# Performance work log

Measured on AMD Instinct MI355X. Metric: run time of the kernel, lower is better.

## Reference

```python
import jax, jax.numpy as jnp
import numpy as np

D_MODEL = 2048
N_HEAD = 16
HEAD_DIM = D_MODEL // N_HEAD
SCALE = 1.0 / (HEAD_DIM ** 0.5)


def setup_inputs() -> dict:
    key = jax.random.key(0)
    kx, kq, kk, kv, ko = jax.random.split(key, 5)
    std = 1.0 / np.sqrt(D_MODEL)
    return {
        "x": jax.random.normal(kx, (2, 2048, D_MODEL), dtype=jnp.float32),
        "w_q": jax.random.normal(kq, (D_MODEL, D_MODEL), dtype=jnp.float32) * std,
        "w_k": jax.random.normal(kk, (D_MODEL, D_MODEL), dtype=jnp.float32) * std,
        "w_v": jax.random.normal(kv, (D_MODEL, D_MODEL), dtype=jnp.float32) * std,
        "w_o": jax.random.normal(ko, (D_MODEL, D_MODEL), dtype=jnp.float32) * std,
    }


def reference(x, w_q, w_k, w_v, w_o):
    b, s, d = x.shape
    # nn.Linear(d,d,bias=False): y = x @ W^T, weights stored [out, in]
    def proj(w):
        y = jnp.einsum("bsd,ed->bse", x, w)
        return y.reshape(b, s, N_HEAD, HEAD_DIM).transpose(0, 2, 1, 3)  # [b,h,s,hd]
    q, k, v = proj(w_q), proj(w_k), proj(w_v)
    scores = jnp.einsum("bhqd,bhkd->bhqk", q, k) * SCALE  # [b,h,s,s]
    probs = jax.nn.softmax(scores, axis=-1)
    attn = jnp.einsum("bhqk,bhkd->bhqd", probs, v)
    attn = attn.transpose(0, 2, 1, 3).reshape(b, s, d)
    return jnp.einsum("bsd,ed->bse", attn, w_o)
```

## Files before the change

### kernel.cpp

```cpp
#include <hip/hip_runtime.h>

#define D_MODEL 2048
#define SEQ 2048
#define BATCH 2
#define NH 16
#define HD 128
#define MTOT 4096
#define NQKV 6144
#define QSTRIDE 4096

static constexpr float SCALE_LOG2E = 0.08838834764831845f * 1.4426950408889634f;

typedef __bf16 bf16x8 __attribute__((ext_vector_type(8)));
typedef _Float16 f16x4 __attribute__((ext_vector_type(4)));
typedef float f32x4 __attribute__((ext_vector_type(4)));

__device__ inline unsigned short f2bf(float f) {
  unsigned int u = __builtin_bit_cast(unsigned int, f);
  u += 0x7fffu + ((u >> 16) & 1u);
  return (unsigned short)(u >> 16);
}

__device__ inline float fast_exp2(float x) {
#if __has_builtin(__builtin_amdgcn_exp2f)
  return __builtin_amdgcn_exp2f(x);
#else
  return exp2f(x);
#endif
}

__device__ inline void gload_lds16(const void* g, void* s) {
  __builtin_amdgcn_global_load_lds(
      (__attribute__((address_space(1))) void*)g,
      (__attribute__((address_space(3))) void*)s, 16, 0, 0);
}

__global__ __launch_bounds__(256) void cvt_all(
    const float* __restrict__ x, const float* __restrict__ wq,
    const float* __restrict__ wk, const float* __restrict__ wv,
    const float* __restrict__ wo, unsigned short* __restrict__ xb,
    unsigned short* __restrict__ wqkv, unsigned short* __restrict__ wob) {
  const int y = blockIdx.y;
  const float* src;
  unsigned short* dst;
  int n4;
  if (y == 0) { src = x; dst = xb; n4 = MTOT * D_MODEL / 4; }
  else if (y == 4) { src = wo; dst = wob; n4 = D_MODEL * D_MODEL / 4; }
  else {
    src = (y == 1) ? wq : (y == 2) ? wk : wv;
    dst = wqkv + (size_t)(y - 1) * D_MODEL * D_MODEL;
    n4 = D_MODEL * D_MODEL / 4;
  }
  int i = blockIdx.x * 256 + threadIdx.x;
  if (i < n4) {
    float4 v = ((const float4*)src)[i];
    ushort4 o;
    o.x = f2bf(v.x); o.y = f2bf(v.y); o.z = f2bf(v.z); o.w = f2bf(v.w);
    ((ushort4*)dst)[i] = o;
  }
}

#define GEMM_SETUP(Aptr, Bptr)                                                 \
  const int tid = threadIdx.x;                                                 \
  const int lane = tid & 63;                                                   \
  const int wave = tid >> 6;                                                   \
  const int quad = lane >> 4;                                                  \
  const int l15 = lane & 15;                                                   \
  const int wm = wave >> 1;                                                    \
  const int wn = wave & 1;                                                     \
  const unsigned short* Ag =                                                   \
      (Aptr) + (size_t)(m0 + wave * 8 + (lane >> 3)) * 2048 +                  \
      (size_t)(((lane & 7) ^ (lane >> 3)) * 8);                                \
  const unsigned short* Bg =                                                   \
      (Bptr) + (size_t)(n0 + wave * 8 + (lane >> 3)) * 2048 +                  \
      (size_t)(((lane & 7) ^ (lane >> 3)) * 8);                                \
  char* sd = smem + wave * 1024;                                               \
  const int arow0 = (wm * 64 + l15) * 128;                                     \
  const int brow0 = (wn * 64 + l15) * 128;                                     \
  const int sk0 = ((quad) ^ (l15 & 7)) * 16;                                   \
  const int sk1 = ((4 + quad) ^ (l15 & 7)) * 16;                               \
  f32x4 acc[4][4] = {};

#define SA(tt, u, NB)                                                          \
  gload_lds16(Ag + (size_t)(u) * 64 * 2048 + (tt) * 64,                        \
              sd + (NB) * 49152 + (u) * 8192)
#define SB(tt, u, NB)                                                          \
  gload_lds16(Bg + (size_t)(u) * 64 * 2048 + (tt) * 64,                        \
              sd + (NB) * 49152 + 32768 + (u) * 8192)

#define RDA(dst, mi, CB)                                                       \
  dst[0] = *(const bf16x8*)(smem + (CB) * 49152 + arow0 + (mi) * 2048 + sk0);  \
  dst[1] = *(const bf16x8*)(smem + (CB) * 49152 + arow0 + (mi) * 2048 + sk1);
#define RDB(ni, CB)                                                            \
  bfr[ni][0] =                                                                 \
      *(const bf16x8*)(smem + (CB) * 49152 + 32768 + brow0 + (ni) * 2048 + sk0); \
  bfr[ni][1] =                                                                 \
      *(const bf16x8*)(smem + (CB) * 49152 + 32768 + brow0 + (ni) * 2048 + sk1);

#define MM2(mi, areg)                                                          \
  _Pragma("unroll") for (int ni_ = 0; ni_ < 4; ni_++) {                        \
    acc[mi][ni_] = __builtin_amdgcn_mfma_f32_16x16x32_bf16(                    \
        areg[0], bfr[ni_][0], acc[mi][ni_], 0, 0, 0);                          \
    acc[mi][ni_] = __builtin_amdgcn_mfma_f32_16x16x32_bf16(                    \
        areg[1], bfr[ni_][1], acc[mi][ni_], 0, 0, 0);                          \
  }

#define TILE(t, CB, NB, DOSTAGE, VMN)                                          \
  {                                                                            \
    bf16x8 af0[2], af1[2], af2[2], af3[2], bfr[4][2];                          \
    RDA(af0, 0, CB); RDA(af1, 1, CB);                                          \
    RDB(0, CB); RDB(1, CB); RDB(2, CB); RDB(3, CB);                            \
    if (DOSTAGE) { SA((t) + 2, 0, NB); SA((t) + 2, 1, NB); SB((t) + 2, 0, NB); } \
    __builtin_amdgcn_s_barrier();                                              \
    asm volatile("s_waitcnt lgkmcnt(0)" ::: "memory");                         \
    __builtin_amdgcn_sched_barrier(0);                                         \
    __builtin_amdgcn_s_setprio(1);                                             \
    MM2(0, af0); MM2(1, af1);                                                  \
    __builtin_amdgcn_s_setprio(0);                                             \
    __builtin_amdgcn_s_barrier();                                              \
    RDA(af2, 2, CB); RDA(af3, 3, CB);                                          \
    if (DOSTAGE) { SA((t) + 2, 2, NB); SA((t) + 2, 3, NB); SB((t) + 2, 1, NB); } \
    __builtin_amdgcn_s_barrier();                                              \
    asm volatile("s_waitcnt lgkmcnt(0)" ::: "memory");                         \
    __builtin_amdgcn_sched_barrier(0);                                         \
    __builtin_amdgcn_s_setprio(1);                                             \
    MM2(2, af2); MM2(3, af3);                                                  \
    __builtin_amdgcn_s_setprio(0);                                             \
    asm volatile("s_waitcnt vmcnt(" #VMN ")" ::: "memory");                    \
    __builtin_amdgcn_s_barrier();                                              \
  }

#define GEMM_KLOOP()                                                           \
  SA(0, 0, 0); SA(0, 1, 0); SA(0, 2, 0); SA(0, 3, 0); SB(0, 0, 0); SB(0, 1, 0);\
  SA(1, 0, 1); SA(1, 1, 1); SA(1, 2, 1); SA(1, 3, 1); SB(1, 0, 1); SB(1, 1, 1);\
  asm volatile("s_waitcnt vmcnt(6)" ::: "memory");                             \
  __builtin_amdgcn_s_barrier();                                                \
  for (int t = 0; t < 30; t += 3) {                                            \
    TILE(t + 0, 0, 2, 1, 6);                                                   \
    TILE(t + 1, 1, 0, 1, 6);                                                   \
    TILE(t + 2, 2, 1, 1, 6);                                                   \
  }                                                                            \
  TILE(30, 0, 2, 0, 0);                                                        \
  TILE(31, 1, 0, 0, 0);

__global__ __launch_bounds__(512, 2) void gemm_qkv(
    const unsigned short* __restrict__ A, const unsigned short* __restrict__ B,
    unsigned short* __restrict__ QK, unsigned short* __restrict__ Vt) {
  extern __shared__ __align__(16) char smem[];
  const int bid = blockIdx.x;
  const int wgid = (bid & 7) * 96 + (bid >> 3);
  const int tm = wgid / 48;
  const int tn = wgid - tm * 48;
  const int m0 = tm * 256;
  const int n0 = tn * 128;
  GEMM_SETUP(A, B);
  GEMM_KLOOP();

  if (n0 < 4096) {
#pragma unroll
    for (int mi = 0; mi < 4; mi++)
#pragma unroll
      for (int ni = 0; ni < 4; ni++) {
        const int mm = m0 + wm * 64 + mi * 16 + quad * 4;
        const int nn = n0 + wn * 64 + ni * 16 + l15;
#pragma unroll
        for (int r = 0; r < 4; r++)
          QK[(size_t)(mm + r) * QSTRIDE + nn] = f2bf(acc[mi][ni][r]);
      }
  } else {
    asm volatile("s_waitcnt vmcnt(0)" ::: "memory");
    __builtin_amdgcn_s_barrier();
    unsigned short* T = (unsigned short*)smem;
    const int h = (n0 - 4096) >> 7;
    const int bb = m0 >> 11;
    const int sbase = m0 & (SEQ - 1);
#pragma unroll
    for (int mi = 0; mi < 4; mi++)
#pragma unroll
      for (int ni = 0; ni < 4; ni++) {
        const int d = wn * 64 + ni * 16 + l15;
        const int s = wm * 64 + mi * 16 + quad * 4;
        f16x4 hv;
#pragma unroll
        for (int r = 0; r < 4; r++) hv[r] = (_Float16)acc[mi][ni][r];
        *(f16x4*)(T + d * 264 + s) = hv;
      }
    __builtin_amdgcn_s_barrier();
    const int d = tid >> 2;
    const int sc = (tid & 3) * 64;
    const size_t vrow = ((size_t)(bb * NH + h) * HD + d) * SEQ + sbase + sc;
#pragma unroll
    for (int j = 0; j < 8; j++) {
      float4 c4 = *(const float4*)(T + d * 264 + sc + j * 8);
      *(float4*)(Vt + vrow + j * 8) = c4;
    }
  }
}

__global__ __launch_bounds__(512, 2) void gemm_out(
    const unsigned short* __restrict__ A, const unsigned short* __restrict__ B,
    float* __restrict__ C) {
  extern __shared__ __align__(16) char smem[];
  const int bid = blockIdx.x;
  const int wgid = (bid & 7) * 32 + (bid >> 3);
  const int tm = wgid >> 4;
  const int tn = wgid & 15;
  const int m0 = tm * 256;
  const int n0 = tn * 128;
  GEMM_SETUP(A, B);
  GEMM_KLOOP();

#pragma unroll
  for (int mi = 0; mi < 4; mi++)
#pragma unroll
    for (int ni = 0; ni < 4; ni++) {
      const int mm = m0 + wm * 64 + mi * 16 + quad * 4;
      const int nn = n0 + wn * 64 + ni * 16 + l15;
#pragma unroll
      for (int r = 0; r < 4; r++)
        C[(size_t)(mm + r) * D_MODEL + nn] = acc[mi][ni][r];
    }
}

__global__ __launch_bounds__(256, 2) void flash_attn(
    const unsigned short* __restrict__ QK, const unsigned short* __restrict__ Vt,
    unsigned short* __restrict__ Og) {
  __shared__ __align__(16) unsigned short Ks[2][64 * 128];
  __shared__ __align__(16) unsigned short Vs[2][128 * 64];
  const int tid = threadIdx.x;
  const int lane = tid & 63;
  const int wave = tid >> 6;
  const int quad = lane >> 4;
  const int l15 = lane & 15;
  const int id = blockIdx.x;
  const int xr = id & 7;
  const int kk = id >> 3;
  const int bh = xr * 4 + (kk >> 4);
  const int b = bh >> 4, h = bh & 15;
  const int q0 = (kk & 15) * 128;

  const size_t kbase = (size_t)(b * SEQ) * QSTRIDE + D_MODEL + h * HD;
  const size_t vbase = (size_t)bh * HD * SEQ;

  bf16x8 qf[2][4];
#pragma unroll
  for (int t = 0; t < 2; t++)
#pragma unroll
    for (int kc = 0; kc < 4; kc++)
      qf[t][kc] = *(const bf16x8*)(QK + (size_t)(b * SEQ + q0 + wave * 32 + t * 16 + l15) * QSTRIDE +
                                   h * HD + kc * 32 + quad * 8);

  const unsigned short* kg[4];
  const unsigned short* vg[4];
  int klofs[4], vlofs[4];
#pragma unroll
  for (int i = 0; i < 4; i++) {
    int krow = wave * 16 + i * 4 + quad;
    int kc_ = l15 ^ (i * 4 + quad);
    kg[i] = QK + kbase + (size_t)krow * QSTRIDE + kc_ * 8;
    klofs[i] = (wave * 16 + i * 4) * 128;
    int vrow = wave * 32 + i * 8 + (lane >> 3);
    int vc_ = (lane & 7) ^ (lane >> 3);
    vg[i] = Vt + vbase + (size_t)vrow * SEQ + vc_ * 8;
    vlofs[i] = (wave * 32 + i * 8) * 64;
  }

#pragma unroll
  for (int i = 0; i < 4; i++) gload_lds16(kg[i], &Ks[0][klofs[i]]);
#pragma unroll
  for (int i = 0; i < 4; i++) gload_lds16(vg[i], &Vs[0][vlofs[i]]);
#pragma unroll
  for (int i = 0; i < 4; i++) { kg[i] += 64 * QSTRIDE; vg[i] += 64; }
  __builtin_amdgcn_s_waitcnt(0);
  __syncthreads();

  float lsum[2] = {0.f, 0.f};
  f32x4 Oa[2][8] = {};

  for (int it = 0; it < SEQ / 64; ++it) {
    const int cur = it & 1;
    if (it < SEQ / 64 - 1) {
#pragma unroll
      for (int i = 0; i < 4; i++) gload_lds16(kg[i], &Ks[cur ^ 1][klofs[i]]);
#pragma unroll
      for (int i = 0; i < 4; i++) gload_lds16(vg[i], &Vs[cur ^ 1][vlofs[i]]);
#pragma unroll
      for (int i = 0; i < 4; i++) { kg[i] += 64 * QSTRIDE; vg[i] += 64; }
    }

    const unsigned short* kb = &Ks[cur][0];
    f32x4 sacc[2][4] = {};
#pragma unroll
    for (int js = 0; js < 4; js++)
#pragma unroll
      for (int kc = 0; kc < 4; kc++) {
        bf16x8 kf = *(const bf16x8*)(kb + (js * 16 + l15) * 128 + (((kc * 4 + quad) ^ l15) * 8));
        sacc[0][js] = __builtin_amdgcn_mfma_f32_16x16x32_bf16(kf, qf[0][kc], sacc[0][js], 0, 0, 0);
        sacc[1][js] = __builtin_amdgcn_mfma_f32_16x16x32_bf16(kf, qf[1][kc], sacc[1][js], 0, 0, 0);
      }

    f16x4 pb[2][4];
#pragma unroll
    for (int t = 0; t < 2; t++)
#pragma unroll
      for (int js = 0; js < 4; js++)
#pragma unroll
        for (int r = 0; r < 4; r++) {
          float p = fast_exp2(sacc[t][js][r] * SCALE_LOG2E);
          lsum[t] += p;
          pb[t][js][r] = (_Float16)p;
        }

    const unsigned short* vb_ = &Vs[cur][0];
#pragma unroll
    for (int jt = 0; jt < 8; jt++)
#pragma unroll
      for (int js = 0; js < 4; js++) {
        f16x4 vf = *(const f16x4*)(vb_ + (jt * 16 + l15) * 64 +
                                   (((js * 2 + (quad >> 1)) ^ (lane & 7)) * 8) + (quad & 1) * 4);
        Oa[0][jt] = __builtin_amdgcn_mfma_f32_16x16x16f16(vf, pb[0][js], Oa[0][jt], 0, 0, 0);
        Oa[1][jt] = __builtin_amdgcn_mfma_f32_16x16x16f16(vf, pb[1][js], Oa[1][jt], 0, 0, 0);
      }

    __builtin_amdgcn_s_waitcnt(0);
    __syncthreads();
  }

  float inv[2];
#pragma unroll
  for (int t = 0; t < 2; t++) {
    float s = lsum[t];
    s += __shfl_xor(s, 16);
    s += __shfl_xor(s, 32);
    inv[t] = 1.0f / s;
  }

#pragma unroll
  for (int t = 0; t < 2; t++) {
    const size_t rowbase = (size_t)(b * SEQ + q0 + wave * 32 + t * 16 + l15) * D_MODEL + h * HD;
#pragma unroll
    for (int jt = 0; jt < 8; jt++) {
      ushort4 o;
      o.x = f2bf(Oa[t][jt][0] * inv[t]);
      o.y = f2bf(Oa[t][jt][1] * inv[t]);
      o.z = f2bf(Oa[t][jt][2] * inv[t]);
      o.w = f2bf(Oa[t][jt][3] * inv[t]);
      *(ushort4*)(Og + rowbase + jt * 16 + quad * 4) = o;
    }
  }
}

extern "C" void kernel_launch(void* const* d_in, const int* in_sizes, int n_in,
                              void* d_out, int out_size, void* d_ws, size_t ws_size,
                              hipStream_t stream) {
  const float* x = (const float*)d_in[0];
  const float* wq = (const float*)d_in[1];
  const float* wk = (const float*)d_in[2];
  const float* wv = (const float*)d_in[3];
  const float* wo = (const float*)d_in[4];
  float* out = (float*)d_out;
  char* ws = (char*)d_ws;
  const size_t MB = 1u << 20;
  if (ws_size < 96 * MB) return;

  unsigned short* xb = (unsigned short*)(ws);
  unsigned short* wqkv = (unsigned short*)(ws + 16 * MB);
  unsigned short* wob = (unsigned short*)(ws + 40 * MB);
  unsigned short* QKb = (unsigned short*)(ws + 48 * MB);
  unsigned short* Vtb = (unsigned short*)(ws + 80 * MB);
  unsigned short* Ab = xb;

  static int lds_set = 0;
  if (!lds_set) {
    hipFuncSetAttribute((const void*)gemm_qkv,
                        hipFuncAttributeMaxDynamicSharedMemorySize, 147456);
    hipFuncSetAttribute((const void*)gemm_out,
                        hipFuncAttributeMaxDynamicSharedMemorySize, 147456);
    lds_set = 1;
  }

  cvt_all<<<dim3(8192, 5), 256, 0, stream>>>(x, wq, wk, wv, wo, xb, wqkv, wob);

  gemm_qkv<<<768, 512, 147456, stream>>>(xb, wqkv, QKb, Vtb);

  flash_attn<<<512, 256, 0, stream>>>(QKb, Vtb, Ab);

  gemm_out<<<256, 512, 147456, stream>>>(Ab, wob, out);
}
```

Baseline: 359.9 us.

## Split QKV GEMM into QK and V kernels with new tile shapes

Replaces the single fused QKV GEMM (256x128 tiles, 768 blocks) with two kernels. gemm_qk uses 256x256 tiles and a double-buffered schedule with 8x4 accumulators per wave. gemm_v and gemm_out use 128x256 tiles with a triple-buffered schedule. Larger tiles raise operand reuse per LDS load and improve arithmetic intensity. In exchange there is higher register pressure, an extra kernel launch, and grids of 256 blocks that may leave some compute units less well balanced.

```diff
diff --git a/kernel.cpp b/kernel.cpp
--- a/kernel.cpp
+++ b/kernel.cpp
@@ -34,6 +34,15 @@
       (__attribute__((address_space(1))) void*)g,
       (__attribute__((address_space(3))) void*)s, 16, 0, 0);
 }
+
+#define BARX() __builtin_amdgcn_s_barrier()
+#define PRIO(x) __builtin_amdgcn_s_setprio(x)
+#define LGK0()                                              \
+  do {                                                      \
+    asm volatile("s_waitcnt lgkmcnt(0)" ::: "memory");      \
+    __builtin_amdgcn_sched_barrier(0);                      \
+  } while (0)
+#define VMW(n) asm volatile("s_waitcnt vmcnt(" #n ")" ::: "memory")
 
 __global__ __launch_bounds__(256) void cvt_all(
     const float* __restrict__ x, const float* __restrict__ wq,
@@ -60,140 +69,216 @@
   }
 }
 
-#define GEMM_SETUP(Aptr, Bptr)                                                 \
-  const int tid = threadIdx.x;                                                 \
-  const int lane = tid & 63;                                                   \
-  const int wave = tid >> 6;                                                   \
-  const int quad = lane >> 4;                                                  \
-  const int l15 = lane & 15;                                                   \
-  const int wm = wave >> 1;                                                    \
-  const int wn = wave & 1;                                                     \
-  const unsigned short* Ag =                                                   \
-      (Aptr) + (size_t)(m0 + wave * 8 + (lane >> 3)) * 2048 +                  \
-      (size_t)(((lane & 7) ^ (lane >> 3)) * 8);                                \
-  const unsigned short* Bg =                                                   \
-      (Bptr) + (size_t)(n0 + wave * 8 + (lane >> 3)) * 2048 +                  \
-      (size_t)(((lane & 7) ^ (lane >> 3)) * 8);                                \
-  char* sd = smem + wave * 1024;                                               \
-  const int arow0 = (wm * 64 + l15) * 128;                                     \
-  const int brow0 = (wn * 64 + l15) * 128;                                     \
-  const int sk0 = ((quad) ^ (l15 & 7)) * 16;                                   \
-  const int sk1 = ((4 + quad) ^ (l15 & 7)) * 16;                               \
-  f32x4 acc[4][4] = {};
-
-#define SA(tt, u, NB)                                                          \
-  gload_lds16(Ag + (size_t)(u) * 64 * 2048 + (tt) * 64,                        \
-              sd + (NB) * 49152 + (u) * 8192)
-#define SB(tt, u, NB)                                                          \
-  gload_lds16(Bg + (size_t)(u) * 64 * 2048 + (tt) * 64,                        \
-              sd + (NB) * 49152 + 32768 + (u) * 8192)
-
-#define RDA(dst, mi, CB)                                                       \
-  dst[0] = *(const bf16x8*)(smem + (CB) * 49152 + arow0 + (mi) * 2048 + sk0);  \
-  dst[1] = *(const bf16x8*)(smem + (CB) * 49152 + arow0 + (mi) * 2048 + sk1);
-#define RDB(ni, CB)                                                            \
-  bfr[ni][0] =                                                                 \
-      *(const bf16x8*)(smem + (CB) * 49152 + 32768 + brow0 + (ni) * 2048 + sk0); \
-  bfr[ni][1] =                                                                 \
-      *(const bf16x8*)(smem + (CB) * 49152 + 32768 + brow0 + (ni) * 2048 + sk1);
-
-#define MM2(mi, areg)                                                          \
-  _Pragma("unroll") for (int ni_ = 0; ni_ < 4; ni_++) {                        \
-    acc[mi][ni_] = __builtin_amdgcn_mfma_f32_16x16x32_bf16(                    \
-        areg[0], bfr[ni_][0], acc[mi][ni_], 0, 0, 0);                          \
-    acc[mi][ni_] = __builtin_amdgcn_mfma_f32_16x16x32_bf16(                    \
-        areg[1], bfr[ni_][1], acc[mi][ni_], 0, 0, 0);                          \
-  }
-
-#define TILE(t, CB, NB, DOSTAGE, VMN)                                          \
-  {                                                                            \
-    bf16x8 af0[2], af1[2], af2[2], af3[2], bfr[4][2];                          \
-    RDA(af0, 0, CB); RDA(af1, 1, CB);                                          \
-    RDB(0, CB); RDB(1, CB); RDB(2, CB); RDB(3, CB);                            \
-    if (DOSTAGE) { SA((t) + 2, 0, NB); SA((t) + 2, 1, NB); SB((t) + 2, 0, NB); } \
-    __builtin_amdgcn_s_barrier();                                              \
-    asm volatile("s_waitcnt lgkmcnt(0)" ::: "memory");                         \
-    __builtin_amdgcn_sched_barrier(0);                                         \
-    __builtin_amdgcn_s_setprio(1);                                             \
-    MM2(0, af0); MM2(1, af1);                                                  \
-    __builtin_amdgcn_s_setprio(0);                                             \
-    __builtin_amdgcn_s_barrier();                                              \
-    RDA(af2, 2, CB); RDA(af3, 3, CB);                                          \
-    if (DOSTAGE) { SA((t) + 2, 2, NB); SA((t) + 2, 3, NB); SB((t) + 2, 1, NB); } \
-    __builtin_amdgcn_s_barrier();                                              \
-    asm volatile("s_waitcnt lgkmcnt(0)" ::: "memory");                         \
-    __builtin_amdgcn_sched_barrier(0);                                         \
-    __builtin_amdgcn_s_setprio(1);                                             \
-    MM2(2, af2); MM2(3, af3);                                                  \
-    __builtin_amdgcn_s_setprio(0);                                             \
-    asm volatile("s_waitcnt vmcnt(" #VMN ")" ::: "memory");                    \
-    __builtin_amdgcn_s_barrier();                                              \
-  }
-
-#define GEMM_KLOOP()                                                           \
-  SA(0, 0, 0); SA(0, 1, 0); SA(0, 2, 0); SA(0, 3, 0); SB(0, 0, 0); SB(0, 1, 0);\
-  SA(1, 0, 1); SA(1, 1, 1); SA(1, 2, 1); SA(1, 3, 1); SB(1, 0, 1); SB(1, 1, 1);\
-  asm volatile("s_waitcnt vmcnt(6)" ::: "memory");                             \
-  __builtin_amdgcn_s_barrier();                                                \
-  for (int t = 0; t < 30; t += 3) {                                            \
-    TILE(t + 0, 0, 2, 1, 6);                                                   \
-    TILE(t + 1, 1, 0, 1, 6);                                                   \
-    TILE(t + 2, 2, 1, 1, 6);                                                   \
-  }                                                                            \
-  TILE(30, 0, 2, 0, 0);                                                        \
-  TILE(31, 1, 0, 0, 0);
-
-__global__ __launch_bounds__(512, 2) void gemm_qkv(
+__global__ __launch_bounds__(512, 2) void gemm_qk(
     const unsigned short* __restrict__ A, const unsigned short* __restrict__ B,
-    unsigned short* __restrict__ QK, unsigned short* __restrict__ Vt) {
+    unsigned short* __restrict__ QK) {
   extern __shared__ __align__(16) char smem[];
+  const int tid = threadIdx.x;
+  const int lane = tid & 63;
+  const int wave = tid >> 6;
+  const int quad = lane >> 4;
+  const int l15 = lane & 15;
   const int bid = blockIdx.x;
-  const int wgid = (bid & 7) * 96 + (bid >> 3);
-  const int tm = wgid / 48;
-  const int tn = wgid - tm * 48;
-  const int m0 = tm * 256;
-  const int n0 = tn * 128;
-  GEMM_SETUP(A, B);
-  GEMM_KLOOP();
-
-  if (n0 < 4096) {
-#pragma unroll
-    for (int mi = 0; mi < 4; mi++)
-#pragma unroll
-      for (int ni = 0; ni < 4; ni++) {
-        const int mm = m0 + wm * 64 + mi * 16 + quad * 4;
-        const int nn = n0 + wn * 64 + ni * 16 + l15;
-#pragma unroll
-        for (int r = 0; r < 4; r++)
-          QK[(size_t)(mm + r) * QSTRIDE + nn] = f2bf(acc[mi][ni][r]);
-      }
-  } else {
-    asm volatile("s_waitcnt vmcnt(0)" ::: "memory");
-    __builtin_amdgcn_s_barrier();
-    unsigned short* T = (unsigned short*)smem;
-    const int h = (n0 - 4096) >> 7;
-    const int bb = m0 >> 11;
-    const int sbase = m0 & (SEQ - 1);
-#pragma unroll
-    for (int mi = 0; mi < 4; mi++)
-#pragma unroll
-      for (int ni = 0; ni < 4; ni++) {
-        const int d = wn * 64 + ni * 16 + l15;
-        const int s = wm * 64 + mi * 16 + quad * 4;
-        f16x4 hv;
-#pragma unroll
-        for (int r = 0; r < 4; r++) hv[r] = (_Float16)acc[mi][ni][r];
-        *(f16x4*)(T + d * 264 + s) = hv;
-      }
-    __builtin_amdgcn_s_barrier();
-    const int d = tid >> 2;
-    const int sc = (tid & 3) * 64;
-    const size_t vrow = ((size_t)(bb * NH + h) * HD + d) * SEQ + sbase + sc;
-#pragma unroll
-    for (int j = 0; j < 8; j++) {
-      float4 c4 = *(const float4*)(T + d * 264 + sc + j * 8);
-      *(float4*)(Vt + vrow + j * 8) = c4;
+  const int wgid = (bid & 7) * 32 + (bid >> 3);
+  const int tm = wgid >> 4, tn = wgid & 15;
+  const int m0 = tm * 256, n0 = tn * 256;
+  const int wm = wave >> 2;
+  const int wn = wave & 3;
+
+  const unsigned short* Ag = A + (size_t)(m0 + wave * 8 + (lane >> 3)) * 2048 +
+                             (((lane & 7) ^ (lane >> 3)) * 8);
+  const unsigned short* Bg = B + (size_t)(n0 + wave * 8 + (lane >> 3)) * 2048 +
+                             (((lane & 7) ^ (lane >> 3)) * 8);
+  char* sd = smem + wave * 1024;
+
+  const int arow0 = (wm * 128 + l15) * 128;
+  const int brow0 = (wn * 64 + l15) * 128;
+  const int sk0 = (quad ^ (l15 & 7)) * 16;
+  const int sk1 = ((4 + quad) ^ (l15 & 7)) * 16;
+
+  f32x4 acc[8][4] = {};
+  bf16x8 a[4][2], bl[2][2], bh[2][2];
+
+#define QSA(u, nb, ko) \
+  gload_lds16(Ag + (size_t)(u) * 64 * 2048 + (ko), sd + (nb) * 65536 + (u) * 8192)
+#define QSB(u, nb, ko) \
+  gload_lds16(Bg + (size_t)(u) * 64 * 2048 + (ko), sd + (nb) * 65536 + 32768 + (u) * 8192)
+#define QRA(mh, cb)                                                               \
+  _Pragma("unroll") for (int mi = 0; mi < 4; mi++) {                              \
+    a[mi][0] = *(const bf16x8*)(smem + (cb) * 65536 + arow0 + ((mh) * 64 + mi * 16) * 128 + sk0); \
+    a[mi][1] = *(const bf16x8*)(smem + (cb) * 65536 + arow0 + ((mh) * 64 + mi * 16) * 128 + sk1); \
+  }
+#define QRB(dst, nh, cb)                                                          \
+  _Pragma("unroll") for (int ni = 0; ni < 2; ni++) {                              \
+    dst[ni][0] = *(const bf16x8*)(smem + (cb) * 65536 + 32768 + brow0 + ((nh) * 32 + ni * 16) * 128 + sk0); \
+    dst[ni][1] = *(const bf16x8*)(smem + (cb) * 65536 + 32768 + brow0 + ((nh) * 32 + ni * 16) * 128 + sk1); \
+  }
+#define QMM(mh, bsrc, nh)                                                         \
+  _Pragma("unroll") for (int mi = 0; mi < 4; mi++)                                \
+  _Pragma("unroll") for (int ni = 0; ni < 2; ni++) {                              \
+    acc[(mh) * 4 + mi][(nh) * 2 + ni] = __builtin_amdgcn_mfma_f32_16x16x32_bf16(  \
+        a[mi][0], bsrc[ni][0], acc[(mh) * 4 + mi][(nh) * 2 + ni], 0, 0, 0);       \
+    acc[(mh) * 4 + mi][(nh) * 2 + ni] = __builtin_amdgcn_mfma_f32_16x16x32_bf16(  \
+        a[mi][1], bsrc[ni][1], acc[(mh) * 4 + mi][(nh) * 2 + ni], 0, 0, 0);       \
+  }
+
+  QSB(0, 0, 0); QSB(1, 0, 0); QSB(2, 0, 0); QSB(3, 0, 0);
+  QSA(0, 0, 0); QSA(2, 0, 0); QSA(1, 0, 0); QSA(3, 0, 0);
+  VMW(0);
+  BARX();
+
+#define QKTILE(t, cb, nb)                                                         \
+  {                                                                               \
+    const int ko = (((t) + 1) & 31) * 64;                                         \
+                                                                         \
+    QRA(0, cb); QRB(bl, 0, cb);                                                   \
+    QSB(0, nb, ko); QSB(1, nb, ko);                                               \
+    BARX(); LGK0(); PRIO(1); QMM(0, bl, 0); PRIO(0); BARX();                      \
+                                                                         \
+    QRB(bh, 1, cb);                                                               \
+    QSB(2, nb, ko); QSB(3, nb, ko);                                               \
+    BARX(); LGK0(); PRIO(1); QMM(0, bh, 1); PRIO(0); VMW(4); BARX();              \
+                                                                         \
+    QRA(1, cb);                                                                   \
+    QSA(0, nb, ko); QSA(2, nb, ko);                                               \
+    BARX(); LGK0(); PRIO(1); QMM(1, bl, 0); PRIO(0); BARX();                      \
+                                                                         \
+    QSA(1, nb, ko); QSA(3, nb, ko);                                               \
+    PRIO(1); QMM(1, bh, 1); PRIO(0); VMW(2); BARX();                              \
+  }
+
+  for (int t = 0; t < 32; t += 2) {
+    QKTILE(t, 0, 1);
+    QKTILE(t + 1, 1, 0);
+  }
+
+#pragma unroll
+  for (int mi = 0; mi < 8; mi++)
+#pragma unroll
+    for (int ni = 0; ni < 4; ni++) {
+      const int mm = m0 + wm * 128 + mi * 16 + quad * 4;
+      const int nn = n0 + wn * 64 + ni * 16 + l15;
+#pragma unroll
+      for (int r = 0; r < 4; r++)
+        QK[(size_t)(mm + r) * QSTRIDE + nn] = f2bf(acc[mi][ni][r]);
     }
+#undef QSA
+#undef QSB
+#undef QRA
+#undef QRB
+#undef QMM
+#undef QKTILE
+}
+
+#define VCORE_BODY(Aptr, Bptr)                                                    \
+  const int tid = threadIdx.x;                                                    \
+  const int lane = tid & 63;                                                      \
+  const int wave = tid >> 6;                                                      \
+  const int quad = lane >> 4;                                                     \
+  const int l15 = lane & 15;                                                      \
+  const int bid = blockIdx.x;                                                     \
+  const int wgid = (bid & 7) * 32 + (bid >> 3);                                   \
+  const int tm = wgid >> 3, tn = wgid & 7;                                        \
+  const int m0 = tm * 128, n0 = tn * 256;                                         \
+  const int wm = wave >> 1;                                             \
+  const int wn = wave & 1;                                              \
+  const unsigned short* Ag = (Aptr) + (size_t)(m0 + wave * 8 + (lane >> 3)) * 2048 + \
+                             (((lane & 7) ^ (lane >> 3)) * 8);                    \
+  const unsigned short* Bg = (Bptr) + (size_t)(n0 + wave * 8 + (lane >> 3)) * 2048 + \
+                             (((lane & 7) ^ (lane >> 3)) * 8);                    \
+  char* sd = smem + wave * 1024;                                                  \
+  const int arow0 = (wm * 32 + l15) * 128;                                        \
+  const int brow0 = (wn * 128 + l15) * 128;                                       \
+  const int sk0 = (quad ^ (l15 & 7)) * 16;                                        \
+  const int sk1 = ((4 + quad) ^ (l15 & 7)) * 16;                                  \
+  f32x4 acc[2][8] = {};                                                           \
+  bf16x8 a[2][2], bl[4][2], bh[4][2];
+
+#define VSA(u, nb, ko) \
+  gload_lds16(Ag + (size_t)(u) * 64 * 2048 + (ko), sd + (nb) * 49152 + (u) * 8192)
+#define VSB(u, nb, ko) \
+  gload_lds16(Bg + (size_t)(u) * 64 * 2048 + (ko), sd + (nb) * 49152 + 16384 + (u) * 8192)
+#define VRA(cb)                                                                   \
+  _Pragma("unroll") for (int mi = 0; mi < 2; mi++) {                              \
+    a[mi][0] = *(const bf16x8*)(smem + (cb) * 49152 + arow0 + mi * 2048 + sk0);   \
+    a[mi][1] = *(const bf16x8*)(smem + (cb) * 49152 + arow0 + mi * 2048 + sk1);   \
+  }
+#define VRB(dst, nh, cb)                                                          \
+  _Pragma("unroll") for (int ni = 0; ni < 4; ni++) {                              \
+    dst[ni][0] = *(const bf16x8*)(smem + (cb) * 49152 + 16384 + brow0 + ((nh) * 64 + ni * 16) * 128 + sk0); \
+    dst[ni][1] = *(const bf16x8*)(smem + (cb) * 49152 + 16384 + brow0 + ((nh) * 64 + ni * 16) * 128 + sk1); \
+  }
+#define VMM(bsrc, nh)                                                             \
+  _Pragma("unroll") for (int mi = 0; mi < 2; mi++)                                \
+  _Pragma("unroll") for (int ni = 0; ni < 4; ni++) {                              \
+    acc[mi][(nh) * 4 + ni] = __builtin_amdgcn_mfma_f32_16x16x32_bf16(             \
+        a[mi][0], bsrc[ni][0], acc[mi][(nh) * 4 + ni], 0, 0, 0);                  \
+    acc[mi][(nh) * 4 + ni] = __builtin_amdgcn_mfma_f32_16x16x32_bf16(             \
+        a[mi][1], bsrc[ni][1], acc[mi][(nh) * 4 + ni], 0, 0, 0);                  \
+  }
+#define VSTAGE6(nb, ko)                                                           \
+  VSA(0, nb, ko); VSA(1, nb, ko); VSB(0, nb, ko);                                 \
+  VSB(1, nb, ko); VSB(2, nb, ko); VSB(3, nb, ko);
+
+#define VTILE(t, cb, nb)                                                          \
+  {                                                                               \
+    const int ko = (((t) + 2) & 31) * 64;                                         \
+                                                                         \
+    VRA(cb); VRB(bl, 0, cb);                                                      \
+    VSA(0, nb, ko); VSA(1, nb, ko); VSB(0, nb, ko);                               \
+    BARX(); LGK0(); PRIO(1); VMM(bl, 0); PRIO(0); BARX();                         \
+                                                                         \
+    VRB(bh, 1, cb);                                                               \
+    VSB(1, nb, ko); VSB(2, nb, ko); VSB(3, nb, ko);                               \
+    BARX(); LGK0(); PRIO(1); VMM(bh, 1); PRIO(0); VMW(6); BARX();                 \
+  }
+
+#define VCORE_LOOP()                                                              \
+  VSTAGE6(0, 0);                                                                  \
+  VSTAGE6(1, 64);                                                                 \
+  VMW(6);                                                                         \
+  BARX();                                                                         \
+  for (int t = 0; t < 30; t += 3) {                                               \
+    VTILE(t + 0, 0, 2);                                                           \
+    VTILE(t + 1, 1, 0);                                                           \
+    VTILE(t + 2, 2, 1);                                                           \
+  }                                                                               \
+  VTILE(30, 0, 2);                                                                \
+  VTILE(31, 1, 0);
+
+__global__ __launch_bounds__(512, 2) void gemm_v(
+    const unsigned short* __restrict__ A, const unsigned short* __restrict__ B,
+    unsigned short* __restrict__ Vt) {
+  extern __shared__ __align__(16) char smem[];
+  VCORE_BODY(A, B);
+  VCORE_LOOP();
+
+  VMW(0);
+  BARX();
+  unsigned short* T = (unsigned short*)smem;
+  const int h0 = n0 >> 7;
+  const int bb = m0 >> 11;
+  const int sbase = m0 & (SEQ - 1);
+#pragma unroll
+  for (int mi = 0; mi < 2; mi++)
+#pragma unroll
+    for (int q = 0; q < 8; q++) {
+      const int d = q * 16 + l15;
+      const int slocal = wm * 32 + mi * 16 + quad * 4;
+      f16x4 hv;
+#pragma unroll
+      for (int r = 0; r < 4; r++) hv[r] = (_Float16)acc[mi][q][r];
+      *(f16x4*)(T + wn * 17408 + d * 136 + slocal) = hv;
+    }
+  BARX();
+  const int hd2 = tid >> 8;
+  const int d = (tid >> 1) & 127;
+  const int sc = (tid & 1) * 64;
+  const size_t vrow = ((size_t)((bb * NH + h0 + hd2) * HD + d)) * SEQ + sbase + sc;
+#pragma unroll
+  for (int j = 0; j < 8; j++) {
+    float4 c4 = *(const float4*)(T + hd2 * 17408 + d * 136 + sc + j * 8);
+    *(float4*)(Vt + vrow + j * 8) = c4;
   }
 }
 
@@ -201,24 +286,18 @@
     const unsigned short* __restrict__ A, const unsigned short* __restrict__ B,
     float* __restrict__ C) {
   extern __shared__ __align__(16) char smem[];
-  const int bid = blockIdx.x;
-  const int wgid = (bid & 7) * 32 + (bid >> 3);
-  const int tm = wgid >> 4;
-  const int tn = wgid & 15;
-  const int m0 = tm * 256;
-  const int n0 = tn * 128;
-  GEMM_SETUP(A, B);
-  GEMM_KLOOP();
-
-#pragma unroll
-  for (int mi = 0; mi < 4; mi++)
-#pragma unroll
-    for (int ni = 0; ni < 4; ni++) {
-      const int mm = m0 + wm * 64 + mi * 16 + quad * 4;
-      const int nn = n0 + wn * 64 + ni * 16 + l15;
+  VCORE_BODY(A, B);
+  VCORE_LOOP();
+
+#pragma unroll
+  for (int mi = 0; mi < 2; mi++)
+#pragma unroll
+    for (int q = 0; q < 8; q++) {
+      const int mm = m0 + wm * 32 + mi * 16 + quad * 4;
+      const int nn = n0 + wn * 128 + q * 16 + l15;
 #pragma unroll
       for (int r = 0; r < 4; r++)
-        C[(size_t)(mm + r) * D_MODEL + nn] = acc[mi][ni][r];
+        C[(size_t)(mm + r) * D_MODEL + nn] = acc[mi][q][r];
     }
 }
 
@@ -372,7 +451,9 @@
 
   static int lds_set = 0;
   if (!lds_set) {
-    hipFuncSetAttribute((const void*)gemm_qkv,
+    hipFuncSetAttribute((const void*)gemm_qk,
+                        hipFuncAttributeMaxDynamicSharedMemorySize, 131072);
+    hipFuncSetAttribute((const void*)gemm_v,
                         hipFuncAttributeMaxDynamicSharedMemorySize, 147456);
     hipFuncSetAttribute((const void*)gemm_out,
                         hipFuncAttributeMaxDynamicSharedMemorySize, 147456);
@@ -381,7 +462,8 @@
 
   cvt_all<<<dim3(8192, 5), 256, 0, stream>>>(x, wq, wk, wv, wo, xb, wqkv, wob);
 
-  gemm_qkv<<<768, 512, 147456, stream>>>(xb, wqkv, QKb, Vtb);
+  gemm_qk<<<256, 512, 131072, stream>>>(xb, wqkv, QKb);
+  gemm_v<<<256, 512, 147456, stream>>>(xb, wqkv + (size_t)4096 * 2048, Vtb);
 
   flash_attn<<<512, 256, 0, stream>>>(QKb, Vtb, Ab);
 
```

After: 355.5 us. No clear change (-1.2%).
